# Optimization experiments

Hardware: AMD Instinct MI355X
Metric: run time of the kernel (lower is better)

Reference implementation:

```python
import jax, jax.numpy as jnp
import numpy as np

B, S, D_IN, D_HEAD = 4, 4096, 1024, 64

def setup_inputs() -> dict:
    key = jax.random.key(0)
    k1, k2, k3, k4 = jax.random.split(key, 4)
    scale = 0.02
    return {
        "input_vectors": jax.random.normal(k1, (B, S, D_IN), dtype=jnp.float32),
        "Wq": jax.random.normal(k2, (D_IN, D_HEAD), dtype=jnp.float32) * scale,
        "Wk": jax.random.normal(k3, (D_IN, D_HEAD), dtype=jnp.float32) * scale,
        "Wv": jax.random.normal(k4, (D_IN, D_HEAD), dtype=jnp.float32) * scale,
    }

def reference(input_vectors, Wq, Wk, Wv):
    # QKV projections (Linear with no bias): [B,S,d_in] @ [d_in,d_head]
    q = input_vectors @ Wq  # [B,S,H]
    k = input_vectors @ Wk
    v = input_vectors @ Wv
    n = input_vectors.shape[1]
    # causal attention scores: [B,S,S]
    scores = jnp.einsum('bqh,bkh->bqk', q, k)
    causal = jnp.tril(jnp.ones((n, n), dtype=bool))  # True = keep
    scores = jnp.where(causal, scores, -jnp.inf)
    scale = k.shape[-1] ** -0.5
    attn = jax.nn.softmax(scores * scale, axis=-1)
    return jnp.einsum('bqk,bkh->bqh', attn, v)
```

## Files before the change

### kernel.cpp

```cpp
#include <hip/hip_runtime.h>
#include <stdint.h>

#define SEQ   4096
#define DIN   1024

typedef __attribute__((ext_vector_type(8))) short bf16x8;
typedef __attribute__((ext_vector_type(4))) float floatx4;
typedef __attribute__((ext_vector_type(4))) unsigned short ushortx4;

#if __has_builtin(__builtin_amdgcn_exp2f)
#define EXP2(x) __builtin_amdgcn_exp2f(x)
#else
#define EXP2(x) exp2f(x)
#endif

__device__ __forceinline__ unsigned short f2bf(float f) {
    union { float f; unsigned int u; } v; v.f = f;
    unsigned int u = v.u + 0x7fffu + ((v.u >> 16) & 1u);
    return (unsigned short)(u >> 16);
}
__device__ __forceinline__ float bf2f(unsigned short h) {
    union { unsigned int u; float f; } v; v.u = ((unsigned int)h) << 16;
    return v.f;
}
__device__ __forceinline__ float uasf(unsigned int u) {
    union { unsigned int u; float f; } v; v.u = u; return v.f;
}
__device__ __forceinline__ unsigned int fasu(float f) {
    union { float f; unsigned int u; } v; v.f = f; return v.u;
}
__device__ __forceinline__ float dpp_xor1(float x) {
    return uasf((unsigned)__builtin_amdgcn_mov_dpp((int)fasu(x), 0xB1, 0xF, 0xF, true));
}
__device__ __forceinline__ float dpp_xor2(float x) {
    return uasf((unsigned)__builtin_amdgcn_mov_dpp((int)fasu(x), 0x4E, 0xF, 0xF, true));
}

__global__ void wt_prep(const float* __restrict__ Wq, const float* __restrict__ Wk,
                        const float* __restrict__ Wv, unsigned short* __restrict__ WT) {
    int idx = blockIdx.x * 256 + threadIdx.x;
    int k   = idx & 1023;
    int n   = (idx >> 10) & 63;
    int mat = idx >> 16;
    const float* W = (mat == 0) ? Wq : ((mat == 1) ? Wk : Wv);
    WT[idx] = f2bf(W[k * 64 + n]);
}

#define QSCALE 0.18033688011112042f
__launch_bounds__(512, 2)
__global__ void proj_qkv(const float* __restrict__ X, const unsigned short* __restrict__ WT,
                         unsigned short* __restrict__ qb, unsigned short* __restrict__ kb,
                         unsigned short* __restrict__ vb) {
    __shared__ __align__(16) float          X0[64 * 64], X1[64 * 64];
    __shared__ __align__(16) unsigned short W0[192 * 64], W1[192 * 64];
    const int tid = threadIdx.x;
    const int wave = tid >> 6, lane = tid & 63;
    const int quad = lane >> 4, l16 = lane & 15;
    const int strip = wave >> 1;
    const int cg = wave & 1;
    const int row0 = blockIdx.x * 64;
    const int m = strip * 16 + l16;

    floatx4 acc[6];
#pragma unroll
    for (int i = 0; i < 6; i++) acc[i] = (floatx4){0.f, 0.f, 0.f, 0.f};

    int xu[2], xr[2], xc[2], wu[3], wr[3], wc[3];
#pragma unroll
    for (int i = 0; i < 2; i++) {
        xu[i] = i * 512 + tid; xr[i] = xu[i] >> 4; xc[i] = (xu[i] & 15) ^ (xr[i] & 15);
    }
#pragma unroll
    for (int i = 0; i < 3; i++) {
        wu[i] = i * 512 + tid; wr[i] = wu[i] >> 3; wc[i] = (wu[i] & 7) ^ (wr[i] & 7);
    }
    floatx4 xpre[2], wpre[3];
    auto issue = [&](int k0) {
#pragma unroll
        for (int i = 0; i < 2; i++)
            xpre[i] = *(const floatx4*)(X + (size_t)(row0 + xr[i]) * DIN + k0 + xc[i] * 4);
#pragma unroll
        for (int i = 0; i < 3; i++)
            wpre[i] = *(const floatx4*)(WT + (size_t)wr[i] * 1024 + k0 + wc[i] * 8);
    };

    issue(0);
    for (int kc = 0; kc < 16; kc++) {
        float*          Xd = (kc & 1) ? X1 : X0;
        unsigned short* Wd = (kc & 1) ? W1 : W0;
#pragma unroll
        for (int i = 0; i < 2; i++) *(floatx4*)&Xd[xu[i] * 4] = xpre[i];
#pragma unroll
        for (int i = 0; i < 3; i++) *(floatx4*)&Wd[wu[i] * 8] = wpre[i];
        __syncthreads();
        if (kc < 15) issue((kc + 1) * 64);

        bf16x8 af[2];
#pragma unroll
        for (int ks = 0; ks < 2; ks++) {
            floatx4 x0 = *(const floatx4*)&Xd[m * 64 + ((ks * 8 + quad * 2 + 0) ^ (m & 15)) * 4];
            floatx4 x1 = *(const floatx4*)&Xd[m * 64 + ((ks * 8 + quad * 2 + 1) ^ (m & 15)) * 4];
#pragma unroll
            for (int j = 0; j < 4; j++) {
                af[ks][j]     = (short)f2bf(x0[j]);
                af[ks][j + 4] = (short)f2bf(x1[j]);
            }
        }
#pragma unroll
        for (int i = 0; i < 6; i++) {
            const int nrow = (cg * 6 + i) * 16 + l16;
#pragma unroll
            for (int ks = 0; ks < 2; ks++) {
                const int c = ks * 4 + quad;
                bf16x8 bfrag = *(const bf16x8*)&Wd[nrow * 64 + (c ^ (nrow & 7)) * 8];
                acc[i] = __builtin_amdgcn_mfma_f32_16x16x32_bf16(af[ks], bfrag, acc[i], 0, 0, 0);
            }
        }
    }
#pragma unroll
    for (int i = 0; i < 6; i++) {
        const int nt = cg * 6 + i;
        const int mat = nt >> 2;
        const int col = (nt & 3) * 16 + l16;
#pragma unroll
        for (int r = 0; r < 4; r++) {
            const int orow = row0 + strip * 16 + quad * 4 + r;
            float v = acc[i][r];
            if (mat == 0) {
                qb[(size_t)orow * 64 + col] = f2bf(v * QSCALE);
            } else if (mat == 1) {
                kb[(size_t)orow * 64 + col] = f2bf(v);
            } else {
                int b = orow >> 12, sq = orow & 4095;
                vb[((size_t)b * 64 + col) * SEQ + sq] = f2bf(v);
            }
        }
    }
}

__launch_bounds__(256, 4)
__global__ void attn(const unsigned short* __restrict__ qb, const unsigned short* __restrict__ kb,
                     const unsigned short* __restrict__ vb, unsigned short* __restrict__ opart,
                     float* __restrict__ lpart) {
    __shared__ __align__(16) unsigned short Kl[64 * 64];
    __shared__ __align__(16) unsigned short Vl[64 * 64];
    __shared__ __align__(16) unsigned short Pl[4][16 * 72];

    const int bid = blockIdx.x;
    const int qt = 63 - (bid >> 4);
    const int batch = (bid >> 2) & 3;
    const int s = bid & 3;
    const int q0 = qt * 64;
    const int T = qt + 1;
    const int lo = (T * s) >> 2, hi = (T * (s + 1)) >> 2;

    const int tid = threadIdx.x;
    const int wave = tid >> 6, lane = tid & 63;
    const int quad = lane >> 4, l16 = lane & 15;

    const unsigned short* qr = qb + (size_t)(batch * SEQ + q0 + wave * 16 + l16) * 64;
    bf16x8 qa0 = *(const bf16x8*)(qr + quad * 8);
    bf16x8 qa1 = *(const bf16x8*)(qr + 32 + quad * 8);

    floatx4 o[4];
#pragma unroll
    for (int i = 0; i < 4; i++) o[i] = (floatx4){0.f, 0.f, 0.f, 0.f};
    float lsum = 0.f;

    const unsigned short* kbase = kb + (size_t)batch * SEQ * 64;
    const unsigned short* vbase = vb + (size_t)batch * 64 * SEQ;
    unsigned short* P = &Pl[wave][0];

    int ku[2], kr[2], kc_[2], vu[2], vd[2], vc[2];
#pragma unroll
    for (int i = 0; i < 2; i++) {
        ku[i] = i * 256 + tid; kr[i] = ku[i] >> 3; kc_[i] = (ku[i] & 7) ^ (kr[i] & 7);
        vu[i] = i * 256 + tid; vd[i] = vu[i] >> 3; vc[i] = (vu[i] & 7) ^ (vd[i] & 7);
    }
    floatx4 kpre[2], vpre[2];
    auto issue = [&](int k0) {
#pragma unroll
        for (int i = 0; i < 2; i++)
            kpre[i] = *(const floatx4*)(kbase + (size_t)(k0 + kr[i]) * 64 + kc_[i] * 8);
#pragma unroll
        for (int i = 0; i < 2; i++)
            vpre[i] = *(const floatx4*)(vbase + (size_t)vd[i] * SEQ + k0 + vc[i] * 8);
    };

    if (lo < hi) issue(lo * 64);
    for (int kt = lo; kt < hi; kt++) {
        __syncthreads();
#pragma unroll
        for (int i = 0; i < 2; i++) *(floatx4*)&Kl[ku[i] * 8] = kpre[i];
#pragma unroll
        for (int i = 0; i < 2; i++) *(floatx4*)&Vl[vu[i] * 8] = vpre[i];
        __syncthreads();
        if (kt + 1 < hi) issue((kt + 1) * 64);

        const int k0 = kt * 64;
        floatx4 sc[4];
#pragma unroll
        for (int nt = 0; nt < 4; nt++) {
            sc[nt] = (floatx4){0.f, 0.f, 0.f, 0.f};
            const int key = nt * 16 + l16;
#pragma unroll
            for (int ks = 0; ks < 2; ks++) {
                const int c = ks * 4 + quad;
                bf16x8 bk = *(const bf16x8*)&Kl[key * 64 + (c ^ (key & 7)) * 8];
                sc[nt] = __builtin_amdgcn_mfma_f32_16x16x32_bf16(
                    ks == 0 ? qa0 : qa1, bk, sc[nt], 0, 0, 0);
            }
        }
        if (kt == T - 1) {
#pragma unroll
            for (int nt = 0; nt < 4; nt++) {
                const int col = k0 + nt * 16 + l16;
#pragma unroll
                for (int r = 0; r < 4; r++) {
                    const int rowg = q0 + wave * 16 + quad * 4 + r;
                    if (col > rowg) sc[nt][r] = -1e30f;
                }
            }
        }
#pragma unroll
        for (int nt = 0; nt < 4; nt++) {
            float v0 = EXP2(sc[nt][0]), v1 = EXP2(sc[nt][1]);
            float v2 = EXP2(sc[nt][2]), v3 = EXP2(sc[nt][3]);
            float t0 = dpp_xor2(v0), t1 = dpp_xor2(v1), t2 = dpp_xor2(v2), t3 = dpp_xor2(v3);
            if (lane & 2) { v0 = t2; v1 = t3; } else { v2 = t0; v3 = t1; }
            t0 = dpp_xor1(v0); t1 = dpp_xor1(v1); t2 = dpp_xor1(v2); t3 = dpp_xor1(v3);
            if (lane & 1) { v0 = t1; v2 = t3; } else { v1 = t0; v3 = t2; }
            unsigned int u0 = fasu(v0) & 0xffff0000u, u1 = fasu(v1) & 0xffff0000u;
            unsigned int u2 = fasu(v2) & 0xffff0000u, u3 = fasu(v3) & 0xffff0000u;
            lsum += (uasf(u0) + uasf(u1)) + (uasf(u2) + uasf(u3));
            uint2 w;
            w.x = (u0 >> 16) | u1;
            w.y = (u2 >> 16) | u3;
            const int prow = quad * 4 + (lane & 3);
            const int pcol = nt * 16 + (l16 >> 2) * 4;
            *(uint2*)&P[prow * 72 + pcol] = w;
        }
#pragma unroll
        for (int ks = 0; ks < 2; ks++) {
            bf16x8 pa = *(const bf16x8*)&P[l16 * 72 + ks * 32 + quad * 8];
#pragma unroll
            for (int nt = 0; nt < 4; nt++) {
                const int d = nt * 16 + l16;
                bf16x8 bv = *(const bf16x8*)&Vl[d * 64 + ((ks * 4 + quad) ^ (d & 7)) * 8];
                o[nt] = __builtin_amdgcn_mfma_f32_16x16x32_bf16(pa, bv, o[nt], 0, 0, 0);
            }
        }
    }

    unsigned short* ob = opart + (size_t)s * (4 * SEQ * 64)
                       + (size_t)(batch * SEQ + q0 + wave * 16) * 64;
    float* lb = lpart + (size_t)s * (4 * SEQ) + (batch * SEQ + q0 + wave * 16);
    float l = lsum;
    l += __shfl_xor(l, 4);
    l += __shfl_xor(l, 8);
#pragma unroll
    for (int nt = 0; nt < 4; nt++)
#pragma unroll
        for (int r = 0; r < 4; r++)
            ob[(quad * 4 + r) * 64 + nt * 16 + l16] = f2bf(o[nt][r]);
    if ((l16 >> 2) == 0) lb[quad * 4 + (lane & 3)] = l;
}

__global__ void merge(const unsigned short* __restrict__ opart, const float* __restrict__ lpart,
                      float* __restrict__ out) {
    int idx = blockIdx.x * 256 + threadIdx.x;
    int row = idx >> 4, c4 = idx & 15;
    float l = lpart[row] + lpart[4 * SEQ + row] + lpart[8 * SEQ + row] + lpart[12 * SEQ + row];
    float inv = 1.f / l;
    floatx4 acc = (floatx4){0.f, 0.f, 0.f, 0.f};
#pragma unroll
    for (int s = 0; s < 4; s++) {
        ushortx4 u = *(const ushortx4*)(opart + (size_t)s * (4 * SEQ * 64)
                                        + (size_t)row * 64 + c4 * 4);
#pragma unroll
        for (int j = 0; j < 4; j++) acc[j] += bf2f(u[j]);
    }
    acc *= inv;
    *(floatx4*)(out + (size_t)row * 64 + c4 * 4) = acc;
}

extern "C" void kernel_launch(void* const* d_in, const int* in_sizes, int n_in,
                              void* d_out, int out_size, void* d_ws, size_t ws_size,
                              hipStream_t stream) {
    const float* X  = (const float*)d_in[0];
    const float* Wq = (const float*)d_in[1];
    const float* Wk = (const float*)d_in[2];
    const float* Wv = (const float*)d_in[3];
    float* out = (float*)d_out;
    char* ws = (char*)d_ws;
    unsigned short* WT    = (unsigned short*)(ws + 0);
    unsigned short* qb    = (unsigned short*)(ws + 393216);
    unsigned short* kb    = (unsigned short*)(ws + 2490368);
    unsigned short* vb    = (unsigned short*)(ws + 4587520);
    unsigned short* opart = (unsigned short*)(ws + 6684672);
    float*          lpart = (float*)(ws + 15073280);

    hipLaunchKernelGGL(wt_prep,  dim3(768),  dim3(256), 0, stream, Wq, Wk, Wv, WT);
    hipLaunchKernelGGL(proj_qkv, dim3(256),  dim3(512), 0, stream, X, WT, qb, kb, vb);
    hipLaunchKernelGGL(attn,     dim3(1024), dim3(256), 0, stream, qb, kb, vb, opart, lpart);
    hipLaunchKernelGGL(merge,    dim3(1024), dim3(256), 0, stream, opart, lpart, out);
}
```

Baseline: 136.9 us.

## Split QKV projection across three blocks per row tile and pin prefetch scheduling

The projection kernel now launches three 256-thread blocks per 64-row tile, one each for Q, K and V, instead of one 512-thread block computing all three. Each block uses single-buffered LDS with smaller tiles, which gives more blocks and more occupancy on the GPU. The cost is that every X tile is read from global memory three times. Sched barriers are also placed before the next-tile prefetch in both the projection and attention loops, so the compiler cannot reorder the loads across them.

New measurement: 141.9 us. 1.04x slower.

```diff
diff --git a/kernel.cpp b/kernel.cpp
--- a/kernel.cpp
+++ b/kernel.cpp
@@ -47,59 +47,60 @@
 }
 
 #define QSCALE 0.18033688011112042f
-__launch_bounds__(512, 2)
+__launch_bounds__(256, 4)
 __global__ void proj_qkv(const float* __restrict__ X, const unsigned short* __restrict__ WT,
                          unsigned short* __restrict__ qb, unsigned short* __restrict__ kb,
                          unsigned short* __restrict__ vb) {
-    __shared__ __align__(16) float          X0[64 * 64], X1[64 * 64];
-    __shared__ __align__(16) unsigned short W0[192 * 64], W1[192 * 64];
+    __shared__ __align__(16) float          Xl[64 * 64];
+    __shared__ __align__(16) unsigned short Wl[64 * 64];
     const int tid = threadIdx.x;
     const int wave = tid >> 6, lane = tid & 63;
     const int quad = lane >> 4, l16 = lane & 15;
-    const int strip = wave >> 1;
-    const int cg = wave & 1;
-    const int row0 = blockIdx.x * 64;
-    const int m = strip * 16 + l16;
-
-    floatx4 acc[6];
-#pragma unroll
-    for (int i = 0; i < 6; i++) acc[i] = (floatx4){0.f, 0.f, 0.f, 0.f};
-
-    int xu[2], xr[2], xc[2], wu[3], wr[3], wc[3];
+    const int rt = blockIdx.x / 3, ch = blockIdx.x % 3;
+    const int row0 = rt * 64;
+    const int m = wave * 16 + l16;
+
+    floatx4 acc[4];
+#pragma unroll
+    for (int i = 0; i < 4; i++) acc[i] = (floatx4){0.f, 0.f, 0.f, 0.f};
+
+    int xu[4], xr[4], xc[4], wu[2], wr[2], wc[2];
+#pragma unroll
+    for (int i = 0; i < 4; i++) {
+        xu[i] = i * 256 + tid; xr[i] = xu[i] >> 4; xc[i] = (xu[i] & 15) ^ (xr[i] & 15);
+    }
 #pragma unroll
     for (int i = 0; i < 2; i++) {
-        xu[i] = i * 512 + tid; xr[i] = xu[i] >> 4; xc[i] = (xu[i] & 15) ^ (xr[i] & 15);
-    }
-#pragma unroll
-    for (int i = 0; i < 3; i++) {
-        wu[i] = i * 512 + tid; wr[i] = wu[i] >> 3; wc[i] = (wu[i] & 7) ^ (wr[i] & 7);
-    }
-    floatx4 xpre[2], wpre[3];
+        wu[i] = i * 256 + tid; wr[i] = wu[i] >> 3; wc[i] = (wu[i] & 7) ^ (wr[i] & 7);
+    }
+    floatx4 xpre[4], wpre[2];
     auto issue = [&](int k0) {
 #pragma unroll
+        for (int i = 0; i < 4; i++)
+            xpre[i] = *(const floatx4*)(X + (size_t)(row0 + xr[i]) * DIN + k0 + xc[i] * 4);
+#pragma unroll
         for (int i = 0; i < 2; i++)
-            xpre[i] = *(const floatx4*)(X + (size_t)(row0 + xr[i]) * DIN + k0 + xc[i] * 4);
-#pragma unroll
-        for (int i = 0; i < 3; i++)
-            wpre[i] = *(const floatx4*)(WT + (size_t)wr[i] * 1024 + k0 + wc[i] * 8);
+            wpre[i] = *(const floatx4*)(WT + (size_t)(ch * 64 + wr[i]) * 1024 + k0 + wc[i] * 8);
     };
 
     issue(0);
     for (int kc = 0; kc < 16; kc++) {
-        float*          Xd = (kc & 1) ? X1 : X0;
-        unsigned short* Wd = (kc & 1) ? W1 : W0;
-#pragma unroll
-        for (int i = 0; i < 2; i++) *(floatx4*)&Xd[xu[i] * 4] = xpre[i];
-#pragma unroll
-        for (int i = 0; i < 3; i++) *(floatx4*)&Wd[wu[i] * 8] = wpre[i];
+        if (kc > 0) __syncthreads();
+#pragma unroll
+        for (int i = 0; i < 4; i++) *(floatx4*)&Xl[xu[i] * 4] = xpre[i];
+#pragma unroll
+        for (int i = 0; i < 2; i++) *(floatx4*)&Wl[wu[i] * 8] = wpre[i];
         __syncthreads();
-        if (kc < 15) issue((kc + 1) * 64);
+        if (kc < 15) {
+            __builtin_amdgcn_sched_barrier(0);
+            issue((kc + 1) * 64);
+        }
 
         bf16x8 af[2];
 #pragma unroll
         for (int ks = 0; ks < 2; ks++) {
-            floatx4 x0 = *(const floatx4*)&Xd[m * 64 + ((ks * 8 + quad * 2 + 0) ^ (m & 15)) * 4];
-            floatx4 x1 = *(const floatx4*)&Xd[m * 64 + ((ks * 8 + quad * 2 + 1) ^ (m & 15)) * 4];
+            floatx4 x0 = *(const floatx4*)&Xl[m * 64 + ((ks * 8 + quad * 2 + 0) ^ (m & 15)) * 4];
+            floatx4 x1 = *(const floatx4*)&Xl[m * 64 + ((ks * 8 + quad * 2 + 1) ^ (m & 15)) * 4];
 #pragma unroll
             for (int j = 0; j < 4; j++) {
                 af[ks][j]     = (short)f2bf(x0[j]);
@@ -107,28 +108,26 @@
             }
         }
 #pragma unroll
-        for (int i = 0; i < 6; i++) {
-            const int nrow = (cg * 6 + i) * 16 + l16;
+        for (int i = 0; i < 4; i++) {
+            const int nrow = i * 16 + l16;
 #pragma unroll
             for (int ks = 0; ks < 2; ks++) {
                 const int c = ks * 4 + quad;
-                bf16x8 bfrag = *(const bf16x8*)&Wd[nrow * 64 + (c ^ (nrow & 7)) * 8];
+                bf16x8 bfrag = *(const bf16x8*)&Wl[nrow * 64 + (c ^ (nrow & 7)) * 8];
                 acc[i] = __builtin_amdgcn_mfma_f32_16x16x32_bf16(af[ks], bfrag, acc[i], 0, 0, 0);
             }
         }
     }
 #pragma unroll
-    for (int i = 0; i < 6; i++) {
-        const int nt = cg * 6 + i;
-        const int mat = nt >> 2;
-        const int col = (nt & 3) * 16 + l16;
+    for (int i = 0; i < 4; i++) {
+        const int col = i * 16 + l16;
 #pragma unroll
         for (int r = 0; r < 4; r++) {
-            const int orow = row0 + strip * 16 + quad * 4 + r;
+            const int orow = row0 + wave * 16 + quad * 4 + r;
             float v = acc[i][r];
-            if (mat == 0) {
+            if (ch == 0) {
                 qb[(size_t)orow * 64 + col] = f2bf(v * QSCALE);
-            } else if (mat == 1) {
+            } else if (ch == 1) {
                 kb[(size_t)orow * 64 + col] = f2bf(v);
             } else {
                 int b = orow >> 12, sq = orow & 4095;
@@ -195,7 +194,10 @@
 #pragma unroll
         for (int i = 0; i < 2; i++) *(floatx4*)&Vl[vu[i] * 8] = vpre[i];
         __syncthreads();
-        if (kt + 1 < hi) issue((kt + 1) * 64);
+        if (kt + 1 < hi) {
+            __builtin_amdgcn_sched_barrier(0);
+            issue((kt + 1) * 64);
+        }
 
         const int k0 = kt * 64;
         floatx4 sc[4];
@@ -301,7 +303,7 @@
     float*          lpart = (float*)(ws + 15073280);
 
     hipLaunchKernelGGL(wt_prep,  dim3(768),  dim3(256), 0, stream, Wq, Wk, Wv, WT);
-    hipLaunchKernelGGL(proj_qkv, dim3(256),  dim3(512), 0, stream, X, WT, qb, kb, vb);
+    hipLaunchKernelGGL(proj_qkv, dim3(768),  dim3(256), 0, stream, X, WT, qb, kb, vb);
     hipLaunchKernelGGL(attn,     dim3(1024), dim3(256), 0, stream, qb, kb, vb, opart, lpart);
     hipLaunchKernelGGL(merge,    dim3(1024), dim3(256), 0, stream, opart, lpart, out);
 }
```

## Fuse split-K merge into attention via atomic last-block reduction

Applied to the files above, without the earlier changes.

Removes the separate merge kernel: each attention block bumps a per-(batch, q-tile) atomic counter after writing its partial output, and the fourth block to finish reduces the four partials and writes the final output. It also reorders the block-index mapping so splits alternate the q-tile direction, balancing causal work across the grid. It moves the next-tile prefetch issue ahead of the barrier in both the projection and attention loops so loads overlap the sync. The cost is a memset launch, atomics and fences, and a serialized tail reduction done by one block per tile.

Measured after the change: 204.0 us. +49.0%, slower.

```diff
diff --git a/kernel.cpp b/kernel.cpp
--- a/kernel.cpp
+++ b/kernel.cpp
@@ -92,8 +92,8 @@
         for (int i = 0; i < 2; i++) *(floatx4*)&Xd[xu[i] * 4] = xpre[i];
 #pragma unroll
         for (int i = 0; i < 3; i++) *(floatx4*)&Wd[wu[i] * 8] = wpre[i];
+        if (kc < 15) issue((kc + 1) * 64);
         __syncthreads();
-        if (kc < 15) issue((kc + 1) * 64);
 
         bf16x8 af[2];
 #pragma unroll
@@ -141,15 +141,20 @@
 __launch_bounds__(256, 4)
 __global__ void attn(const unsigned short* __restrict__ qb, const unsigned short* __restrict__ kb,
                      const unsigned short* __restrict__ vb, unsigned short* __restrict__ opart,
-                     float* __restrict__ lpart) {
+                     float* __restrict__ lpart, unsigned int* __restrict__ cnt,
+                     float* __restrict__ out) {
     __shared__ __align__(16) unsigned short Kl[64 * 64];
     __shared__ __align__(16) unsigned short Vl[64 * 64];
     __shared__ __align__(16) unsigned short Pl[4][16 * 72];
+    __shared__ int lastflag;
 
     const int bid = blockIdx.x;
-    const int qt = 63 - (bid >> 4);
-    const int batch = (bid >> 2) & 3;
-    const int s = bid & 3;
+    const int z = bid >> 8;
+    const int y = bid & 255;
+    const int batch = y >> 6;
+    const int mq = y & 63;
+    const int qt = (z & 1) ? (63 - mq) : mq;
+    const int s = z;
     const int q0 = qt * 64;
     const int T = qt + 1;
     const int lo = (T * s) >> 2, hi = (T * (s + 1)) >> 2;
@@ -194,8 +199,8 @@
         for (int i = 0; i < 2; i++) *(floatx4*)&Kl[ku[i] * 8] = kpre[i];
 #pragma unroll
         for (int i = 0; i < 2; i++) *(floatx4*)&Vl[vu[i] * 8] = vpre[i];
+        if (kt + 1 < hi) issue((kt + 1) * 64);
         __syncthreads();
-        if (kt + 1 < hi) issue((kt + 1) * 64);
 
         const int k0 = kt * 64;
         floatx4 sc[4];
@@ -264,24 +269,33 @@
         for (int r = 0; r < 4; r++)
             ob[(quad * 4 + r) * 64 + nt * 16 + l16] = f2bf(o[nt][r]);
     if ((l16 >> 2) == 0) lb[quad * 4 + (lane & 3)] = l;
-}
-
-__global__ void merge(const unsigned short* __restrict__ opart, const float* __restrict__ lpart,
-                      float* __restrict__ out) {
-    int idx = blockIdx.x * 256 + threadIdx.x;
-    int row = idx >> 4, c4 = idx & 15;
-    float l = lpart[row] + lpart[4 * SEQ + row] + lpart[8 * SEQ + row] + lpart[12 * SEQ + row];
-    float inv = 1.f / l;
-    floatx4 acc = (floatx4){0.f, 0.f, 0.f, 0.f};
-#pragma unroll
-    for (int s = 0; s < 4; s++) {
-        ushortx4 u = *(const ushortx4*)(opart + (size_t)s * (4 * SEQ * 64)
-                                        + (size_t)row * 64 + c4 * 4);
-#pragma unroll
-        for (int j = 0; j < 4; j++) acc[j] += bf2f(u[j]);
-    }
-    acc *= inv;
-    *(floatx4*)(out + (size_t)row * 64 + c4 * 4) = acc;
+
+    __syncthreads();
+    if (tid == 0) {
+        __threadfence();
+        unsigned int old = __hip_atomic_fetch_add(&cnt[batch * 64 + qt], 1u,
+                                                  __ATOMIC_ACQ_REL, __HIP_MEMORY_SCOPE_AGENT);
+        lastflag = (old == 3u);
+    }
+    __syncthreads();
+    if (lastflag) {
+        for (int u = tid; u < 1024; u += 256) {
+            const int row = u >> 4, c4 = u & 15;
+            const int grow = batch * SEQ + q0 + row;
+            float lt = lpart[grow] + lpart[4 * SEQ + grow]
+                     + lpart[8 * SEQ + grow] + lpart[12 * SEQ + grow];
+            floatx4 acc = (floatx4){0.f, 0.f, 0.f, 0.f};
+#pragma unroll
+            for (int sp = 0; sp < 4; sp++) {
+                ushortx4 v = *(const ushortx4*)(opart + (size_t)sp * (4 * SEQ * 64)
+                                                + (size_t)grow * 64 + c4 * 4);
+#pragma unroll
+                for (int j = 0; j < 4; j++) acc[j] += bf2f(v[j]);
+            }
+            acc *= (1.f / lt);
+            *(floatx4*)(out + (size_t)grow * 64 + c4 * 4) = acc;
+        }
+    }
 }
 
 extern "C" void kernel_launch(void* const* d_in, const int* in_sizes, int n_in,
@@ -299,9 +313,11 @@
     unsigned short* vb    = (unsigned short*)(ws + 4587520);
     unsigned short* opart = (unsigned short*)(ws + 6684672);
     float*          lpart = (float*)(ws + 15073280);
-
+    unsigned int*   cnt   = (unsigned int*)(ws + 15335424);
+
+    hipMemsetAsync(cnt, 0, 1024, stream);
     hipLaunchKernelGGL(wt_prep,  dim3(768),  dim3(256), 0, stream, Wq, Wk, Wv, WT);
     hipLaunchKernelGGL(proj_qkv, dim3(256),  dim3(512), 0, stream, X, WT, qb, kb, vb);
-    hipLaunchKernelGGL(attn,     dim3(1024), dim3(256), 0, stream, qb, kb, vb, opart, lpart);
-    hipLaunchKernelGGL(merge,    dim3(1024), dim3(256), 0, stream, opart, lpart, out);
-}
+    hipLaunchKernelGGL(attn,     dim3(1024), dim3(256), 0, stream, qb, kb, vb,
+                       opart, lpart, cnt, out);
+}
```
